# Kernel tuning notes

Hardware: AMD Instinct MI355X
Metric: run time of the kernel (lower is better)

Reference implementation:

```python
import jax, jax.numpy as jnp
import numpy as np

H_IMG, W_IMG = 16, 64
HK, WK = 7, 11
DIM, NUM_HEADS = 384, 8
BATCH = 32
SEQ = H_IMG * W_IMG  # 1024


def build_local_mask():
    # Faithful to the torch constructor: for each query position (i,j), a
    # (hk x wk) window of zeros in a padded canvas; everything else -inf.
    h, w, hk, wk = H_IMG, W_IMG, HK, WK
    mask = np.ones((h * w, h + hk - 1, w + wk - 1), dtype=np.float32)
    for i in range(h):
        for j in range(w):
            mask[w * i + j, i:i + hk, j:j + wk] = 0.0
    mask_c = mask[:, hk // 2:h + hk // 2, wk // 2:w + wk // 2].reshape(h * w, h * w)
    out = np.where(mask_c == 1.0, np.float32(-np.inf), mask_c).astype(np.float32)
    return jnp.asarray(out)  # [S, S]


def setup_inputs() -> dict:
    key = jax.random.key(0)
    k1, k2, k3, k4 = jax.random.split(key, 4)
    s = 1.0 / np.sqrt(DIM)
    return {
        "x": jax.random.normal(k1, (BATCH, SEQ, DIM), dtype=jnp.float32),
        "w_qkv": jax.random.normal(k2, (DIM, 3 * DIM), dtype=jnp.float32) * s,
        "w_proj": jax.random.normal(k3, (DIM, DIM), dtype=jnp.float32) * s,
        "b_proj": jax.random.normal(k4, (DIM,), dtype=jnp.float32) * 0.01,
        "mask": build_local_mask(),
    }


def reference(x, w_qkv, w_proj, b_proj, mask):
    B, S, C = x.shape
    H = NUM_HEADS
    D = C // H
    scale = D ** -0.5
    qkv = (x @ w_qkv).reshape(B, S, 3, H, D)
    qkv = jnp.transpose(qkv, (2, 0, 3, 1, 4))  # [3, B, H, S, D]
    q, k, v = qkv[0] * scale, qkv[1], qkv[2]
    attn = jnp.einsum("bhsd,bhtd->bhst", q, k)  # [B, H, S, S]
    attn = attn + mask[None, None]               # additive local-window bias
    attn = jax.nn.softmax(attn, axis=-1)
    out = jnp.einsum("bhst,bhtd->bhsd", attn, v)
    out = jnp.transpose(out, (0, 2, 1, 3)).reshape(B, S, C)
    return out @ w_proj + b_proj
```

## Files before the change

kernel.cpp:

```cpp
#include <hip/hip_runtime.h>
#include <hip/hip_bf16.h>


typedef __attribute__((ext_vector_type(8))) unsigned short ushort8;
typedef __attribute__((ext_vector_type(4))) unsigned short ushort4v;
typedef __attribute__((ext_vector_type(8))) short short8v;
typedef __attribute__((ext_vector_type(4))) float floatx4;

__device__ __forceinline__ float bf2f(unsigned short u) {
  union { unsigned int i; float f; } x;
  x.i = ((unsigned int)u) << 16;
  return x.f;
}

__device__ __forceinline__ unsigned short f2bu(float f) {
  union { float f; unsigned int i; } x;
  x.f = f;
  unsigned int lsb = (x.i >> 16) & 1u;
  x.i += 0x7FFFu + lsb;
  return (unsigned short)(x.i >> 16);
}

__device__ __forceinline__ void gload_lds16(const void* g, void* l) {
  __builtin_amdgcn_global_load_lds(
      (const __attribute__((address_space(1))) unsigned int*)g,
      (__attribute__((address_space(3))) unsigned int*)l, 16, 0, 0);
}

__global__ __launch_bounds__(256) void cvt_f32_bf16(
    const float4* __restrict__ in, ushort4v* __restrict__ out, int n4) {
  const int i = blockIdx.x * 256 + threadIdx.x;
  if (i < n4) {
    const float4 v = in[i];
    ushort4v o;
    o[0] = f2bu(v.x); o[1] = f2bu(v.y); o[2] = f2bu(v.z); o[3] = f2bu(v.w);
    out[i] = o;
  }
}

__global__ __launch_bounds__(256) void transpose_cvt(
    const float* __restrict__ in, unsigned short* __restrict__ out, int R, int C) {
  __shared__ float t[32][33];
  const int c0 = blockIdx.x * 32, r0 = blockIdx.y * 32;
  const int tx = threadIdx.x, ty = threadIdx.y;
  #pragma unroll
  for (int rr = ty; rr < 32; rr += 8) t[rr][tx] = in[(size_t)(r0 + rr) * C + c0 + tx];
  __syncthreads();
  #pragma unroll
  for (int rr = ty; rr < 32; rr += 8)
    out[(size_t)(c0 + rr) * R + r0 + tx] = f2bu(t[tx][rr]);
}

template <int MODE>
__global__ __launch_bounds__(256) void gemm_mfma(
    const unsigned short* __restrict__ A,
    const unsigned short* __restrict__ Bt,
    const float* __restrict__ bias, float* __restrict__ outf,
    unsigned short* __restrict__ qws, unsigned short* __restrict__ kws,
    unsigned short* __restrict__ vtws)
{
  __shared__ unsigned short smem[32768];
  const int tid = threadIdx.x;
  const int lane = tid & 63, w = tid >> 6;
  const int wm = w & 1, wn = w >> 1;

  const int nbx = gridDim.x;
  const int nwg = nbx * gridDim.y;
  const int bid = blockIdx.y * nbx + blockIdx.x;
  const int swz = (bid & 7) * (nwg >> 3) + (bid >> 3);
  const int n0 = (swz % nbx) * 128;
  const int m0 = (swz / nbx) * 128;

  floatx4 acc[4][4];
  #pragma unroll
  for (int mi = 0; mi < 4; ++mi)
    #pragma unroll
    for (int ni = 0; ni < 4; ++ni)
      acc[mi][ni] = (floatx4){0.f, 0.f, 0.f, 0.f};

  const int srow = w * 16 + (lane >> 2);
  const int kslot16 = (lane & 3) * 16;

  auto ASB = [&](int buf) -> unsigned short* { return smem + buf * 4096; };
  auto BSB = [&](int buf) -> unsigned short* { return smem + 16384 + buf * 4096; };

  auto STAGE = [&](int buf, int k0) {
    #pragma unroll
    for (int c = 0; c < 2; ++c) {
      const int r = c * 64 + srow;
      const int kb = kslot16 ^ ((r & 3) << 4);
      gload_lds16((const char*)A + (size_t)(m0 + r) * 768 + k0 * 2 + kb,
                  (char*)ASB(buf) + c * 4096 + w * 1024);
      gload_lds16((const char*)Bt + (size_t)(n0 + r) * 768 + k0 * 2 + kb,
                  (char*)BSB(buf) + c * 4096 + w * 1024);
    }
  };

  auto COMPUTE = [&](int buf) {
    short8v a[4], b[4];
    const int kgb = (lane >> 4) * 16;
    #pragma unroll
    for (int mi = 0; mi < 4; ++mi) {
      const int r = wm * 64 + mi * 16 + (lane & 15);
      a[mi] = *reinterpret_cast<const short8v*>(
          (const char*)ASB(buf) + r * 64 + (kgb ^ ((r & 3) << 4)));
    }
    #pragma unroll
    for (int ni = 0; ni < 4; ++ni) {
      const int r = wn * 64 + ni * 16 + (lane & 15);
      b[ni] = *reinterpret_cast<const short8v*>(
          (const char*)BSB(buf) + r * 64 + (kgb ^ ((r & 3) << 4)));
    }
    #pragma unroll
    for (int mi = 0; mi < 4; ++mi)
      #pragma unroll
      for (int ni = 0; ni < 4; ++ni)
        acc[mi][ni] = __builtin_amdgcn_mfma_f32_16x16x32_bf16(
            a[mi], b[ni], acc[mi][ni], 0, 0, 0);
  };

  STAGE(0, 0);
  STAGE(1, 32);

  #pragma unroll
  for (int s = 0; s < 6; ++s) {
    const int rb = (s & 1) * 2;
    const int sb = rb ^ 2;
    if (s < 5) {
      STAGE(sb, (2 * s + 2) * 32);
      STAGE(sb + 1, (2 * s + 3) * 32);
      asm volatile("s_waitcnt vmcnt(8)" ::: "memory");
    } else {
      asm volatile("s_waitcnt vmcnt(0)" ::: "memory");
    }
    __builtin_amdgcn_s_barrier();
    __builtin_amdgcn_s_setprio(1);
    COMPUTE(rb);
    COMPUTE(rb + 1);
    __builtin_amdgcn_s_setprio(0);
    asm volatile("s_waitcnt lgkmcnt(0)" ::: "memory");
    __builtin_amdgcn_s_barrier();
  }

  const int col_l = lane & 15;
  const int row_l = (lane >> 4) * 4;

  if (MODE == 0) {
    const float QSCALE = 0.14433756729740643f;
    const int which = n0 / 384;
    if (which < 2) {
      unsigned short* dstb = (which == 0) ? qws : kws;
      const float scale = (which == 0) ? QSCALE : 1.f;
      #pragma unroll
      for (int ni = 0; ni < 4; ++ni) {
        const int cg = n0 + wn * 64 + ni * 16 + col_l;
        const int rem = cg - which * 384;
        const int h = rem / 48;
        const int d = rem - h * 48;
        #pragma unroll
        for (int mi = 0; mi < 4; ++mi) {
          #pragma unroll
          for (int reg = 0; reg < 4; ++reg) {
            const int r = m0 + wm * 64 + mi * 16 + row_l + reg;
            const int bb = r >> 10, s = r & 1023;
            dstb[(((size_t)(bb * 8 + h)) * 1024 + s) * 48 + d] =
                f2bu(acc[mi][ni][reg] * scale);
          }
        }
      }
    } else {
      unsigned short* T = smem;
      #pragma unroll
      for (int ni = 0; ni < 4; ++ni) {
        const int col = wn * 64 + ni * 16 + col_l;
        #pragma unroll
        for (int mi = 0; mi < 4; ++mi) {
          const int rowb = wm * 64 + mi * 16 + row_l;
          #pragma unroll
          for (int reg = 0; reg < 4; ++reg)
            T[col * 136 + rowb + reg] = f2bu(acc[mi][ni][reg]);
        }
      }
      __syncthreads();
      const int col = tid >> 1, half = tid & 1;
      const int cg = n0 + col;
      const int rem = cg - 768;
      const int h = rem / 48, d = rem - h * 48;
      const int bb = m0 >> 10;
      const int s0 = (m0 & 1023) + half * 64;
      unsigned short* dst =
          vtws + (((size_t)(bb * 8 + h)) * 48 + d) * 1024 + s0;
      const unsigned short* src = T + col * 136 + half * 64;
      #pragma unroll
      for (int j = 0; j < 8; ++j)
        *reinterpret_cast<ushort8*>(dst + j * 8) =
            *reinterpret_cast<const ushort8*>(src + j * 8);
    }
  } else {
    #pragma unroll
    for (int ni = 0; ni < 4; ++ni) {
      const int cg = n0 + wn * 64 + ni * 16 + col_l;
      const float bv = bias[cg];
      #pragma unroll
      for (int mi = 0; mi < 4; ++mi) {
        #pragma unroll
        for (int reg = 0; reg < 4; ++reg) {
          const int r = m0 + wm * 64 + mi * 16 + row_l + reg;
          outf[(size_t)r * 384 + cg] = acc[mi][ni][reg] + bv;
        }
      }
    }
  }
}

__global__ __launch_bounds__(256) void attn_mfma(
    const unsigned short* __restrict__ qws,
    const unsigned short* __restrict__ kws,
    const unsigned short* __restrict__ vt,
    unsigned short* __restrict__ attn_out)
{
  __shared__ unsigned short plds_all[4 * 64 * 72];

  const int tid = threadIdx.x;
  const int w = tid >> 6;
  const int lane = tid & 63;
  const int blk = blockIdx.x;
  const int sw = ((blk & 7) << 7) | (blk >> 3);
  const int task = sw * 4 + w;
  const int i  = task & 15;
  const int bh = task >> 4;
  const int ql = lane & 15;
  const int g  = lane >> 4;

  unsigned short* plds = plds_all + w * 4608;

  {
    const uint4 zz = make_uint4(0, 0, 0, 0);
    #pragma unroll
    for (int z = 0; z < 9; ++z)
      reinterpret_cast<uint4*>(plds)[lane + z * 64] = zz;
  }

  const unsigned short* qbase = qws + (size_t)bh * 1024 * 48;
  const unsigned short* kbase = kws + (size_t)bh * 1024 * 48;
  const unsigned short* vbase = vt  + (size_t)bh * 48 * 1024;

  const short8v zfrag = (short8v){0, 0, 0, 0, 0, 0, 0, 0};

  short8v qf[4][2];
  #pragma unroll
  for (int qt = 0; qt < 4; ++qt) {
    const unsigned short* qrow = qbase + (size_t)(i * 64 + qt * 16 + ql) * 48;
    qf[qt][0] = *reinterpret_cast<const short8v*>(qrow + 8 * g);
    qf[qt][1] = (g < 2) ? *reinterpret_cast<const short8v*>(qrow + 32 + 8 * g)
                        : zfrag;
  }

  floatx4 ot[3][4];
  #pragma unroll
  for (int dt = 0; dt < 3; ++dt)
    #pragma unroll
    for (int qt = 0; qt < 4; ++qt)
      ot[dt][qt] = (floatx4){0.f, 0.f, 0.f, 0.f};
  float mreg[4] = {-INFINITY, -INFINITY, -INFINITY, -INFINITY};
  float lreg[4] = {0.f, 0.f, 0.f, 0.f};

  const int ki0 = (i - 3 < 0) ? 0 : i - 3;
  const int ki1 = (i + 3 > 15) ? 15 : i + 3;

  for (int ki = ki0; ki <= ki1; ++ki) {
    short8v kf[4][2];
    #pragma unroll
    for (int kt = 0; kt < 4; ++kt) {
      const unsigned short* krow = kbase + (size_t)(ki * 64 + kt * 16 + ql) * 48;
      kf[kt][0] = *reinterpret_cast<const short8v*>(krow + 8 * g);
      kf[kt][1] = (g < 2) ? *reinterpret_cast<const short8v*>(krow + 32 + 8 * g)
                          : zfrag;
    }
    short8v vf[3][2];
    #pragma unroll
    for (int dt = 0; dt < 3; ++dt)
      #pragma unroll
      for (int c = 0; c < 2; ++c)
        vf[dt][c] = *reinterpret_cast<const short8v*>(
            vbase + (size_t)(16 * dt + ql) * 1024 + ki * 64 + 32 * c + 8 * g);

    #pragma unroll
    for (int qt = 0; qt < 4; ++qt) {
      const int kts = (qt == 0) ? 0 : qt - 1;
      const int kte = (qt == 3) ? 3 : qt + 1;
      floatx4 s[4];
      #pragma unroll
      for (int kt = 0; kt < 4; ++kt) {
        if (kt < kts || kt > kte) continue;
        s[kt] = __builtin_amdgcn_mfma_f32_16x16x32_bf16(
            kf[kt][0], qf[qt][0], (floatx4){0.f, 0.f, 0.f, 0.f}, 0, 0, 0);
        s[kt] = __builtin_amdgcn_mfma_f32_16x16x32_bf16(
            kf[kt][1], qf[qt][1], s[kt], 0, 0, 0);
      }
      const int qcol = qt * 16 + ql;
      float pmax = -INFINITY;
      #pragma unroll
      for (int kt = 0; kt < 4; ++kt) {
        if (kt < kts || kt > kte) continue;
        #pragma unroll
        for (int r = 0; r < 4; ++r) {
          const int delta = kt * 16 + 4 * g + r - qcol;
          const bool ok = (delta <= 5) && (delta >= -5);
          s[kt][r] = ok ? s[kt][r] : -INFINITY;
          pmax = fmaxf(pmax, s[kt][r]);
        }
      }
      if (!__all(pmax - mreg[qt] <= 8.0f)) {
        float mt = fmaxf(pmax, __shfl_xor(pmax, 16, 64));
        mt = fmaxf(mt, __shfl_xor(mt, 32, 64));
        const float mnew = fmaxf(mreg[qt], mt);
        const float corr = __expf(mreg[qt] - mnew);
        lreg[qt] *= corr;
        #pragma unroll
        for (int dt = 0; dt < 3; ++dt) {
          ot[dt][qt][0] *= corr; ot[dt][qt][1] *= corr;
          ot[dt][qt][2] *= corr; ot[dt][qt][3] *= corr;
        }
        mreg[qt] = mnew;
      }
      float ps = 0.f;
      #pragma unroll
      for (int kt = 0; kt < 4; ++kt) {
        if (kt < kts || kt > kte) continue;
        #pragma unroll
        for (int r = 0; r < 4; ++r) {
          const float p = __expf(s[kt][r] - mreg[qt]);
          s[kt][r] = p;
          ps += p;
        }
      }
      ps += __shfl_xor(ps, 16, 64);
      ps += __shfl_xor(ps, 32, 64);
      lreg[qt] += ps;
      #pragma unroll
      for (int kt = 0; kt < 4; ++kt) {
        if (kt < kts || kt > kte) continue;
        uint2 pk;
        pk.x = (unsigned int)f2bu(s[kt][0]) | ((unsigned int)f2bu(s[kt][1]) << 16);
        pk.y = (unsigned int)f2bu(s[kt][2]) | ((unsigned int)f2bu(s[kt][3]) << 16);
        *reinterpret_cast<uint2*>(&plds[(qt * 16 + ql) * 72 + kt * 16 + 4 * g]) = pk;
      }
    }

    __builtin_amdgcn_s_setprio(1);
    #pragma unroll
    for (int qt = 0; qt < 4; ++qt) {
      #pragma unroll
      for (int c = 0; c < 2; ++c) {
        const short8v pf = *reinterpret_cast<const short8v*>(
            &plds[(qt * 16 + ql) * 72 + 32 * c + 8 * g]);
        #pragma unroll
        for (int dt = 0; dt < 3; ++dt)
          ot[dt][qt] = __builtin_amdgcn_mfma_f32_16x16x32_bf16(
              vf[dt][c], pf, ot[dt][qt], 0, 0, 0);
      }
    }
    __builtin_amdgcn_s_setprio(0);
  }

  const int b = bh >> 3, h = bh & 7;
  #pragma unroll
  for (int qt = 0; qt < 4; ++qt) {
    const float inv = 1.0f / lreg[qt];
    unsigned short* orow =
        attn_out + (size_t)(b * 1024 + i * 64 + qt * 16 + ql) * 384 + h * 48;
    #pragma unroll
    for (int dt = 0; dt < 3; ++dt) {
      const int d0 = 16 * dt + 4 * g;
      unsigned int w0 = (unsigned int)f2bu(ot[dt][qt][0] * inv) |
                        ((unsigned int)f2bu(ot[dt][qt][1] * inv) << 16);
      unsigned int w1 = (unsigned int)f2bu(ot[dt][qt][2] * inv) |
                        ((unsigned int)f2bu(ot[dt][qt][3] * inv) << 16);
      *reinterpret_cast<unsigned int*>(orow + d0)     = w0;
      *reinterpret_cast<unsigned int*>(orow + d0 + 2) = w1;
    }
  }
}

extern "C" void kernel_launch(void* const* d_in, const int* in_sizes, int n_in,
                              void* d_out, int out_size, void* d_ws, size_t ws_size,
                              hipStream_t stream) {
  const float* x      = (const float*)d_in[0];
  const float* w_qkv  = (const float*)d_in[1];
  const float* w_proj = (const float*)d_in[2];
  const float* b_proj = (const float*)d_in[3];

  const size_t T = 25165824;
  char* ws = (char*)d_ws;
  unsigned short* xb    = (unsigned short*)ws;
  unsigned short* qws   = (unsigned short*)(ws + T);
  unsigned short* kws   = (unsigned short*)(ws + 2 * T);
  unsigned short* vtws  = (unsigned short*)(ws + 3 * T);
  unsigned short* wqkvT = (unsigned short*)(ws + 4 * T);
  unsigned short* wpT   = (unsigned short*)(ws + 4 * T + 884736);
  unsigned short* attn_out = xb;
  float* out = (float*)d_out;

  cvt_f32_bf16<<<12288, 256, 0, stream>>>((const float4*)x, (ushort4v*)xb, 3145728);
  transpose_cvt<<<dim3(36, 12), dim3(32, 8), 0, stream>>>(w_qkv, wqkvT, 384, 1152);
  transpose_cvt<<<dim3(12, 12), dim3(32, 8), 0, stream>>>(w_proj, wpT, 384, 384);

  gemm_mfma<0><<<dim3(9, 256), 256, 0, stream>>>(xb, wqkvT, nullptr, nullptr,
                                                 qws, kws, vtws);
  attn_mfma<<<dim3(1024), 256, 0, stream>>>(qws, kws, vtws, attn_out);
  gemm_mfma<1><<<dim3(3, 256), 256, 0, stream>>>(attn_out, wpT, b_proj, out,
                                                 nullptr, nullptr, nullptr);
}
```

Before: 132.2 us.

## Shrink GEMM LDS pipeline, vectorize Q/K epilogue, skip masked PV MFMAs

The GEMM main loop goes from four 32-wide k-buffers, staged two at a time, to a plain double buffer of single 32-wide stages. This cuts shared memory from 64KB to about 34KB so more workgroups can fit per CU. The Q/K epilogue now transposes through LDS and writes 16-byte vectors instead of scattered 2-byte stores. The attention PV loop also skips the two MFMA chunks that fall fully outside the local window. The tradeoff is shallower prefetch and more barriers per k step.

```diff
diff --git a/kernel.cpp b/kernel.cpp
--- a/kernel.cpp
+++ b/kernel.cpp
@@ -59,7 +59,7 @@
     unsigned short* __restrict__ qws, unsigned short* __restrict__ kws,
     unsigned short* __restrict__ vtws)
 {
-  __shared__ unsigned short smem[32768];
+  __shared__ unsigned short smem[17408];
   const int tid = threadIdx.x;
   const int lane = tid & 63, w = tid >> 6;
   const int wm = w & 1, wn = w >> 1;
@@ -82,7 +82,7 @@
   const int kslot16 = (lane & 3) * 16;
 
   auto ASB = [&](int buf) -> unsigned short* { return smem + buf * 4096; };
-  auto BSB = [&](int buf) -> unsigned short* { return smem + 16384 + buf * 4096; };
+  auto BSB = [&](int buf) -> unsigned short* { return smem + 8192 + buf * 4096; };
 
   auto STAGE = [&](int buf, int k0) {
     #pragma unroll
@@ -120,23 +120,18 @@
   };
 
   STAGE(0, 0);
-  STAGE(1, 32);
-
-  #pragma unroll
-  for (int s = 0; s < 6; ++s) {
-    const int rb = (s & 1) * 2;
-    const int sb = rb ^ 2;
-    if (s < 5) {
-      STAGE(sb, (2 * s + 2) * 32);
-      STAGE(sb + 1, (2 * s + 3) * 32);
-      asm volatile("s_waitcnt vmcnt(8)" ::: "memory");
+
+  for (int t = 0; t < 12; ++t) {
+    const int cur = t & 1;
+    if (t < 11) {
+      STAGE(cur ^ 1, (t + 1) * 32);
+      asm volatile("s_waitcnt vmcnt(4)" ::: "memory");
     } else {
       asm volatile("s_waitcnt vmcnt(0)" ::: "memory");
     }
     __builtin_amdgcn_s_barrier();
     __builtin_amdgcn_s_setprio(1);
-    COMPUTE(rb);
-    COMPUTE(rb + 1);
+    COMPUTE(cur);
     __builtin_amdgcn_s_setprio(0);
     asm volatile("s_waitcnt lgkmcnt(0)" ::: "memory");
     __builtin_amdgcn_s_barrier();
@@ -149,24 +144,34 @@
     const float QSCALE = 0.14433756729740643f;
     const int which = n0 / 384;
     if (which < 2) {
+      unsigned short* T = smem;
+      const float scale = (which == 0) ? QSCALE : 1.f;
+      #pragma unroll
+      for (int ni = 0; ni < 4; ++ni) {
+        const int col = wn * 64 + ni * 16 + col_l;
+        #pragma unroll
+        for (int mi = 0; mi < 4; ++mi) {
+          const int rowb = wm * 64 + mi * 16 + row_l;
+          #pragma unroll
+          for (int reg = 0; reg < 4; ++reg)
+            T[(rowb + reg) * 136 + col] = f2bu(acc[mi][ni][reg] * scale);
+        }
+      }
+      __syncthreads();
       unsigned short* dstb = (which == 0) ? qws : kws;
-      const float scale = (which == 0) ? QSCALE : 1.f;
-      #pragma unroll
-      for (int ni = 0; ni < 4; ++ni) {
-        const int cg = n0 + wn * 64 + ni * 16 + col_l;
-        const int rem = cg - which * 384;
-        const int h = rem / 48;
-        const int d = rem - h * 48;
-        #pragma unroll
-        for (int mi = 0; mi < 4; ++mi) {
-          #pragma unroll
-          for (int reg = 0; reg < 4; ++reg) {
-            const int r = m0 + wm * 64 + mi * 16 + row_l + reg;
-            const int bb = r >> 10, s = r & 1023;
-            dstb[(((size_t)(bb * 8 + h)) * 1024 + s) * 48 + d] =
-                f2bu(acc[mi][ni][reg] * scale);
-          }
-        }
+      const int row = tid >> 1, half = tid & 1;
+      const int s = (m0 & 1023) + row;
+      const int bb = m0 >> 10;
+      const int base_rem = n0 - which * 384;
+      #pragma unroll
+      for (int j = 0; j < 8; ++j) {
+        const int c = half * 64 + j * 8;
+        const int rem = base_rem + c;
+        const int h = rem / 48, d = rem - h * 48;
+        unsigned short* dst =
+            dstb + (((size_t)(bb * 8 + h)) * 1024 + s) * 48 + d;
+        *reinterpret_cast<ushort8*>(dst) =
+            *reinterpret_cast<const ushort8*>(&T[row * 136 + c]);
       }
     } else {
       unsigned short* T = smem;
@@ -353,6 +358,7 @@
     for (int qt = 0; qt < 4; ++qt) {
       #pragma unroll
       for (int c = 0; c < 2; ++c) {
+        if ((qt == 0 && c == 1) || (qt == 3 && c == 0)) continue;
         const short8v pf = *reinterpret_cast<const short8v*>(
             &plds[(qt * 16 + ql) * 72 + 32 * c + 8 * g]);
         #pragma unroll
```

Result: slower. 142.7 us (+8.0%).

## Use 8 waves per GEMM block and skip fully-masked PV MFMA chunks

Applied to the files above, without the earlier changes.

The GEMM kernels now launch 512 threads per 128x128 tile, with 8 waves each computing a 32x64 sub-tile. This halves per-wave accumulators and raises the number of waves available to hide latency. Staging now issues one load per thread per matrix, and the vmcnt wait threshold is adjusted to match. The attention PV loop also skips two P chunks that the local window mask makes entirely zero, relying on the masking geometry being correct.

```diff
diff --git a/kernel.cpp b/kernel.cpp
--- a/kernel.cpp
+++ b/kernel.cpp
@@ -52,7 +52,7 @@
 }
 
 template <int MODE>
-__global__ __launch_bounds__(256) void gemm_mfma(
+__global__ __launch_bounds__(512) void gemm_mfma(
     const unsigned short* __restrict__ A,
     const unsigned short* __restrict__ Bt,
     const float* __restrict__ bias, float* __restrict__ outf,
@@ -62,7 +62,7 @@
   __shared__ unsigned short smem[32768];
   const int tid = threadIdx.x;
   const int lane = tid & 63, w = tid >> 6;
-  const int wm = w & 1, wn = w >> 1;
+  const int wm = w & 3, wn = w >> 2;
 
   const int nbx = gridDim.x;
   const int nwg = nbx * gridDim.y;
@@ -71,48 +71,44 @@
   const int n0 = (swz % nbx) * 128;
   const int m0 = (swz / nbx) * 128;
 
-  floatx4 acc[4][4];
-  #pragma unroll
-  for (int mi = 0; mi < 4; ++mi)
+  floatx4 acc[2][4];
+  #pragma unroll
+  for (int mi = 0; mi < 2; ++mi)
     #pragma unroll
     for (int ni = 0; ni < 4; ++ni)
       acc[mi][ni] = (floatx4){0.f, 0.f, 0.f, 0.f};
 
-  const int srow = w * 16 + (lane >> 2);
-  const int kslot16 = (lane & 3) * 16;
-
-  auto ASB = [&](int buf) -> unsigned short* { return smem + buf * 4096; };
-  auto BSB = [&](int buf) -> unsigned short* { return smem + 16384 + buf * 4096; };
+  const int srow = tid >> 2;
+  const int kslot16 = (tid & 3) * 16;
+
+  auto ASB = [&](int buf) -> char* { return (char*)smem + buf * 8192; };
+  auto BSB = [&](int buf) -> char* { return (char*)smem + 32768 + buf * 8192; };
 
   auto STAGE = [&](int buf, int k0) {
-    #pragma unroll
-    for (int c = 0; c < 2; ++c) {
-      const int r = c * 64 + srow;
-      const int kb = kslot16 ^ ((r & 3) << 4);
-      gload_lds16((const char*)A + (size_t)(m0 + r) * 768 + k0 * 2 + kb,
-                  (char*)ASB(buf) + c * 4096 + w * 1024);
-      gload_lds16((const char*)Bt + (size_t)(n0 + r) * 768 + k0 * 2 + kb,
-                  (char*)BSB(buf) + c * 4096 + w * 1024);
-    }
+    const int kb = kslot16 ^ ((srow & 3) << 4);
+    gload_lds16((const char*)A + (size_t)(m0 + srow) * 768 + k0 * 2 + kb,
+                ASB(buf) + w * 1024);
+    gload_lds16((const char*)Bt + (size_t)(n0 + srow) * 768 + k0 * 2 + kb,
+                BSB(buf) + w * 1024);
   };
 
   auto COMPUTE = [&](int buf) {
-    short8v a[4], b[4];
+    short8v a[2], b[4];
     const int kgb = (lane >> 4) * 16;
     #pragma unroll
-    for (int mi = 0; mi < 4; ++mi) {
-      const int r = wm * 64 + mi * 16 + (lane & 15);
+    for (int mi = 0; mi < 2; ++mi) {
+      const int r = wm * 32 + mi * 16 + (lane & 15);
       a[mi] = *reinterpret_cast<const short8v*>(
-          (const char*)ASB(buf) + r * 64 + (kgb ^ ((r & 3) << 4)));
+          ASB(buf) + r * 64 + (kgb ^ ((r & 3) << 4)));
     }
     #pragma unroll
     for (int ni = 0; ni < 4; ++ni) {
       const int r = wn * 64 + ni * 16 + (lane & 15);
       b[ni] = *reinterpret_cast<const short8v*>(
-          (const char*)BSB(buf) + r * 64 + (kgb ^ ((r & 3) << 4)));
-    }
-    #pragma unroll
-    for (int mi = 0; mi < 4; ++mi)
+          BSB(buf) + r * 64 + (kgb ^ ((r & 3) << 4)));
+    }
+    #pragma unroll
+    for (int mi = 0; mi < 2; ++mi)
       #pragma unroll
       for (int ni = 0; ni < 4; ++ni)
         acc[mi][ni] = __builtin_amdgcn_mfma_f32_16x16x32_bf16(
@@ -129,7 +125,7 @@
     if (s < 5) {
       STAGE(sb, (2 * s + 2) * 32);
       STAGE(sb + 1, (2 * s + 3) * 32);
-      asm volatile("s_waitcnt vmcnt(8)" ::: "memory");
+      asm volatile("s_waitcnt vmcnt(4)" ::: "memory");
     } else {
       asm volatile("s_waitcnt vmcnt(0)" ::: "memory");
     }
@@ -158,10 +154,10 @@
         const int h = rem / 48;
         const int d = rem - h * 48;
         #pragma unroll
-        for (int mi = 0; mi < 4; ++mi) {
+        for (int mi = 0; mi < 2; ++mi) {
           #pragma unroll
           for (int reg = 0; reg < 4; ++reg) {
-            const int r = m0 + wm * 64 + mi * 16 + row_l + reg;
+            const int r = m0 + wm * 32 + mi * 16 + row_l + reg;
             const int bb = r >> 10, s = r & 1023;
             dstb[(((size_t)(bb * 8 + h)) * 1024 + s) * 48 + d] =
                 f2bu(acc[mi][ni][reg] * scale);
@@ -174,25 +170,25 @@
       for (int ni = 0; ni < 4; ++ni) {
         const int col = wn * 64 + ni * 16 + col_l;
         #pragma unroll
-        for (int mi = 0; mi < 4; ++mi) {
-          const int rowb = wm * 64 + mi * 16 + row_l;
+        for (int mi = 0; mi < 2; ++mi) {
+          const int rowb = wm * 32 + mi * 16 + row_l;
           #pragma unroll
           for (int reg = 0; reg < 4; ++reg)
             T[col * 136 + rowb + reg] = f2bu(acc[mi][ni][reg]);
         }
       }
       __syncthreads();
-      const int col = tid >> 1, half = tid & 1;
+      const int col = tid >> 2, q = tid & 3;
       const int cg = n0 + col;
       const int rem = cg - 768;
       const int h = rem / 48, d = rem - h * 48;
       const int bb = m0 >> 10;
-      const int s0 = (m0 & 1023) + half * 64;
+      const int s0 = (m0 & 1023) + q * 32;
       unsigned short* dst =
           vtws + (((size_t)(bb * 8 + h)) * 48 + d) * 1024 + s0;
-      const unsigned short* src = T + col * 136 + half * 64;
-      #pragma unroll
-      for (int j = 0; j < 8; ++j)
+      const unsigned short* src = T + col * 136 + q * 32;
+      #pragma unroll
+      for (int j = 0; j < 4; ++j)
         *reinterpret_cast<ushort8*>(dst + j * 8) =
             *reinterpret_cast<const ushort8*>(src + j * 8);
     }
@@ -202,10 +198,10 @@
       const int cg = n0 + wn * 64 + ni * 16 + col_l;
       const float bv = bias[cg];
       #pragma unroll
-      for (int mi = 0; mi < 4; ++mi) {
+      for (int mi = 0; mi < 2; ++mi) {
         #pragma unroll
         for (int reg = 0; reg < 4; ++reg) {
-          const int r = m0 + wm * 64 + mi * 16 + row_l + reg;
+          const int r = m0 + wm * 32 + mi * 16 + row_l + reg;
           outf[(size_t)r * 384 + cg] = acc[mi][ni][reg] + bv;
         }
       }
@@ -353,6 +349,7 @@
     for (int qt = 0; qt < 4; ++qt) {
       #pragma unroll
       for (int c = 0; c < 2; ++c) {
+        if ((qt == 0 && c == 1) || (qt == 3 && c == 0)) continue;
         const short8v pf = *reinterpret_cast<const short8v*>(
             &plds[(qt * 16 + ql) * 72 + 32 * c + 8 * g]);
         #pragma unroll
@@ -406,9 +403,9 @@
   transpose_cvt<<<dim3(36, 12), dim3(32, 8), 0, stream>>>(w_qkv, wqkvT, 384, 1152);
   transpose_cvt<<<dim3(12, 12), dim3(32, 8), 0, stream>>>(w_proj, wpT, 384, 384);
 
-  gemm_mfma<0><<<dim3(9, 256), 256, 0, stream>>>(xb, wqkvT, nullptr, nullptr,
+  gemm_mfma<0><<<dim3(9, 256), 512, 0, stream>>>(xb, wqkvT, nullptr, nullptr,
                                                  qws, kws, vtws);
   attn_mfma<<<dim3(1024), 256, 0, stream>>>(qws, kws, vtws, attn_out);
-  gemm_mfma<1><<<dim3(3, 256), 256, 0, stream>>>(attn_out, wpT, b_proj, out,
+  gemm_mfma<1><<<dim3(3, 256), 512, 0, stream>>>(attn_out, wpT, b_proj, out,
                                                  nullptr, nullptr, nullptr);
 }
```

After: 131.7 us. About the same (-0.4%).
